# Optimization experiments

Measured on AMD Instinct MI355X. Metric: run time of the kernel, lower is better.

The kernel has to match this reference:

```python
import jax, jax.numpy as jnp
import numpy as np

N_NODES = 100000


def setup_inputs() -> dict:
    key = jax.random.key(0)
    k_x, k_r, k_c, k_v, k_t = jax.random.split(key, 5)
    n_edges = 3200000
    fin, fout = 512, 128
    x = jax.random.normal(k_x, (N_NODES, fin), dtype=jnp.float32)
    rows = jax.random.randint(k_r, (n_edges,), 0, N_NODES, dtype=jnp.int32)
    cols = jax.random.randint(k_c, (n_edges,), 0, N_NODES, dtype=jnp.int32)
    vals = jax.random.uniform(k_v, (n_edges,), dtype=jnp.float32)
    theta = jax.random.normal(k_t, (fin, fout), dtype=jnp.float32) * (1.0 / np.sqrt(fin))
    bias = jnp.zeros((fout,), dtype=jnp.float32)
    return {"x": x, "rows": rows, "cols": cols, "vals": vals, "theta": theta, "bias": bias}


def reference(x, rows, cols, vals, theta, bias):
    # SpMM: mx[i] = sum over edges (i <- j) of A[i,j] * x[j]
    gathered = vals[:, None] * x[cols]                      # [E, fin]
    mx = jax.ops.segment_sum(gathered, rows, num_segments=N_NODES)  # [N, fin]
    # Dense feature transform + bias + relu
    o = jnp.einsum('nf,fo->no', mx, theta) + bias           # [N, fout]
    return jax.nn.relu(o)
```

## Files before the change

### kernel.cpp

```cpp
#include <hip/hip_runtime.h>
#include <stdint.h>
#include <stddef.h>

#define FIN 512
#define FOUT 128
#define BROWS 160
#define NBK 625
#define SORT_CAP 7680
#define TILE 8192

typedef __attribute__((ext_vector_type(8))) short short8;
typedef __attribute__((ext_vector_type(4))) float f32x4;

__device__ __forceinline__ unsigned short f2bf(float f) {
  unsigned u = __builtin_bit_cast(unsigned, f);
  u = (u + 0x7fffu + ((u >> 16) & 1u)) >> 16;
  return (unsigned short)u;
}
__device__ __forceinline__ float bf2f(unsigned short h) {
  unsigned u = ((unsigned)h) << 16;
  return __builtin_bit_cast(float, u);
}

__global__ void prep_theta_k(const float* __restrict__ theta,
                             unsigned short* __restrict__ thetaT) {
  int idx = blockIdx.x * blockDim.x + threadIdx.x;
  int n = idx >> 9;
  int k = idx & 511;
  thetaT[idx] = f2bf(theta[k * FOUT + n]);
}

__global__ __launch_bounds__(256) void gemm_k(const float* __restrict__ x,
                                              const unsigned short* __restrict__ thetaT,
                                              unsigned short* __restrict__ yb, int M) {
  __shared__ __align__(16) unsigned short lA[128 * 40];
  __shared__ __align__(16) unsigned short lB[128 * 40];
  const int tid = threadIdx.x;
  const int row0 = blockIdx.x * 128;
  const int wave = tid >> 6, lane = tid & 63;
  const int wm = wave >> 1, wn = wave & 1;
  const int fr = lane & 15, fq = lane >> 4;
  const int arow = tid >> 1, ahalf = tid & 1;

  f32x4 acc[4][4] = {};

  const int grow = row0 + arow;
  const bool aval = (grow < M);
  const float* asrc = x + (size_t)(aval ? grow : 0) * FIN + ahalf * 16;
  const unsigned short* bsrc = thetaT + (size_t)arow * FIN + ahalf * 16;

  for (int k0 = 0; k0 < FIN; k0 += 32) {
    float av[16];
    if (aval) {
      const float4* p = (const float4*)(asrc + k0);
      float4 v0 = p[0], v1 = p[1], v2 = p[2], v3 = p[3];
      av[0] = v0.x; av[1] = v0.y; av[2] = v0.z; av[3] = v0.w;
      av[4] = v1.x; av[5] = v1.y; av[6] = v1.z; av[7] = v1.w;
      av[8] = v2.x; av[9] = v2.y; av[10] = v2.z; av[11] = v2.w;
      av[12] = v3.x; av[13] = v3.y; av[14] = v3.z; av[15] = v3.w;
    } else {
      for (int i = 0; i < 16; i++) av[i] = 0.f;
    }
    unsigned ap[8];
    for (int i = 0; i < 8; i++)
      ap[i] = (unsigned)f2bf(av[2 * i]) | ((unsigned)f2bf(av[2 * i + 1]) << 16);
    uint4* aw = (uint4*)&lA[arow * 40 + ahalf * 16];
    aw[0] = make_uint4(ap[0], ap[1], ap[2], ap[3]);
    aw[1] = make_uint4(ap[4], ap[5], ap[6], ap[7]);

    const uint4* bp = (const uint4*)(bsrc + k0);
    uint4 b0 = bp[0], b1 = bp[1];
    uint4* bw = (uint4*)&lB[arow * 40 + ahalf * 16];
    bw[0] = b0; bw[1] = b1;

    __syncthreads();

    short8 af[4], bfv[4];
#pragma unroll
    for (int m = 0; m < 4; m++)
      af[m] = *(const short8*)&lA[(wm * 64 + m * 16 + fr) * 40 + fq * 8];
#pragma unroll
    for (int n = 0; n < 4; n++)
      bfv[n] = *(const short8*)&lB[(wn * 64 + n * 16 + fr) * 40 + fq * 8];
#pragma unroll
    for (int m = 0; m < 4; m++)
#pragma unroll
      for (int n = 0; n < 4; n++)
        acc[m][n] = __builtin_amdgcn_mfma_f32_16x16x32_bf16(af[m], bfv[n], acc[m][n], 0, 0, 0);

    __syncthreads();
  }

#pragma unroll
  for (int m = 0; m < 4; m++) {
    int rbase = row0 + wm * 64 + m * 16 + fq * 4;
#pragma unroll
    for (int j = 0; j < 4; j++) {
      int r = rbase + j;
      if (r < M) {
        unsigned short* dst = yb + (size_t)r * FOUT + wn * 64;
#pragma unroll
        for (int n = 0; n < 4; n++) dst[n * 16 + fr] = f2bf(acc[m][n][j]);
      }
    }
  }
}

__global__ __launch_bounds__(256) void tilesort_k(const int* __restrict__ rows,
                                                  const int* __restrict__ cols,
                                                  const float* __restrict__ vals,
                                                  unsigned* __restrict__ rec4tile,
                                                  unsigned char* __restrict__ rlotile,
                                                  int* __restrict__ lofs, int E) {
  __shared__ int hist[NBK];
  __shared__ int wsum[4];
  __shared__ unsigned srec[TILE];
  __shared__ unsigned char srlo[TILE];
  const int c = blockIdx.x, t = threadIdx.x;
  const int base = c * TILE;
  const int n = (E - base < TILE) ? (E - base) : TILE;

  for (int i = t; i < NBK; i += 256) hist[i] = 0;
  __syncthreads();

#pragma unroll
  for (int k = 0; k < TILE / 256; k++) {
    int i = base + k * 256 + t;
    if (i < E) atomicAdd(&hist[rows[i] / BROWS], 1);
  }
  __syncthreads();

  int c0 = t * 3, c1 = c0 + 1, c2 = c0 + 2;
  int h0 = (c0 < NBK) ? hist[c0] : 0;
  int h1 = (c1 < NBK) ? hist[c1] : 0;
  int h2 = (c2 < NBK) ? hist[c2] : 0;
  int loc = h0 + h1 + h2;
  int lane = t & 63, wv = t >> 6;
  int inc = loc;
  for (int off = 1; off < 64; off <<= 1) {
    int u = __shfl_up(inc, off, 64);
    if (lane >= off) inc += u;
  }
  if (lane == 63) wsum[wv] = inc;
  __syncthreads();
  int excl = inc - loc;
  for (int i = 0; i < 4; i++)
    if (i < wv) excl += wsum[i];

  size_t lbase = (size_t)c * (NBK + 1);
  int e = excl;
  if (c0 <= NBK) lofs[lbase + c0] = e;
  __syncthreads();
  if (c0 < NBK) hist[c0] = e;
  e += h0;
  if (c1 <= NBK) lofs[lbase + c1] = e;
  if (c1 < NBK) hist[c1] = e;
  e += h1;
  if (c2 <= NBK) lofs[lbase + c2] = e;
  if (c2 < NBK) hist[c2] = e;
  __syncthreads();

#pragma unroll
  for (int k = 0; k < TILE / 256; k++) {
    int i = base + k * 256 + t;
    if (i < E) {
      int r = rows[i];
      int b = r / BROWS;
      int p = atomicAdd(&hist[b], 1);
      srec[p] = ((unsigned)cols[i] << 15) | ((unsigned)f2bf(vals[i]) & 0x7fffu);
      srlo[p] = (unsigned char)(r - b * BROWS);
    }
  }
  __syncthreads();

  for (int j = t; j < n; j += 256) {
    rec4tile[base + j] = srec[j];
    rlotile[base + j] = srlo[j];
  }
}

__global__ __launch_bounds__(256) void bsum_k(const int* __restrict__ lofs,
                                              int* __restrict__ btotals, int NT) {
  __shared__ int ws[4];
  int b = blockIdx.x, t = threadIdx.x;
  int s = 0;
  for (int c = t; c < NT; c += 256) {
    size_t lb = (size_t)c * (NBK + 1) + b;
    s += lofs[lb + 1] - lofs[lb];
  }
  for (int off = 32; off; off >>= 1) s += __shfl_down(s, off, 64);
  if ((t & 63) == 0) ws[t >> 6] = s;
  __syncthreads();
  if (t == 0) btotals[b] = ws[0] + ws[1] + ws[2] + ws[3];
}

__global__ __launch_bounds__(1024) void bscan_k(const int* __restrict__ btotals,
                                                int* __restrict__ boff,
                                                int* __restrict__ offsets,
                                                int E, int M) {
  __shared__ int tmp[1024];
  int t = threadIdx.x;
  tmp[t] = (t < NBK) ? btotals[t] : 0;
  __syncthreads();
  for (int off = 1; off < 1024; off <<= 1) {
    int v = (t >= off) ? tmp[t - off] : 0;
    __syncthreads();
    tmp[t] += v;
    __syncthreads();
  }
  if (t < NBK) boff[t] = t ? tmp[t - 1] : 0;
  if (t == 0) {
    boff[NBK] = E;
    offsets[M] = E;
  }
}

__global__ __launch_bounds__(256) void bsort_k(const int* __restrict__ boff,
                                               const int* __restrict__ lofs,
                                               const unsigned* __restrict__ rec4tile,
                                               const unsigned char* __restrict__ rlotile,
                                               unsigned* __restrict__ rec4s,
                                               int* __restrict__ offsets,
                                               int NT, int M) {
  __shared__ unsigned s4[SORT_CAP];
  __shared__ unsigned char k8[SORT_CAP];
  __shared__ int lh[256];
  __shared__ int lsc[256];
  __shared__ int wsum[4];
  int b = blockIdx.x, t = threadIdx.x;
  int start = boff[b];

  int ca = 2 * t, cb = 2 * t + 1;
  int la = 0, fa = 0, lb2 = 0, fb = 0;
  if (ca < NT) {
    size_t p = (size_t)ca * (NBK + 1) + b;
    la = lofs[p];
    fa = lofs[p + 1] - la;
  }
  if (cb < NT) {
    size_t p = (size_t)cb * (NBK + 1) + b;
    lb2 = lofs[p];
    fb = lofs[p + 1] - lb2;
  }
  int loc = fa + fb;
  int lane = t & 63, wv = t >> 6;
  int inc = loc;
  for (int off = 1; off < 64; off <<= 1) {
    int u = __shfl_up(inc, off, 64);
    if (lane >= off) inc += u;
  }
  if (lane == 63) wsum[wv] = inc;
  __syncthreads();
  int excl = inc - loc;
  for (int i = 0; i < 4; i++)
    if (i < wv) excl += wsum[i];

  if (ca < NT) {
    const unsigned* src = rec4tile + (size_t)ca * TILE + la;
    const unsigned char* srl = rlotile + (size_t)ca * TILE + la;
    for (int j = 0; j < fa; j++) {
      int d = excl + j;
      if (d < SORT_CAP) { s4[d] = src[j]; k8[d] = srl[j]; }
    }
    excl += fa;
  }
  if (cb < NT) {
    const unsigned* src = rec4tile + (size_t)cb * TILE + lb2;
    const unsigned char* srl = rlotile + (size_t)cb * TILE + lb2;
    for (int j = 0; j < fb; j++) {
      int d = excl + j;
      if (d < SORT_CAP) { s4[d] = src[j]; k8[d] = srl[j]; }
    }
  }

  int n = boff[b + 1] - start;
  if (n > SORT_CAP) n = SORT_CAP;
  lh[t] = 0;
  __syncthreads();

  for (int i = t; i < n; i += 256) atomicAdd(&lh[k8[i]], 1);
  __syncthreads();
  lsc[t] = lh[t];
  __syncthreads();
  for (int off = 1; off < 256; off <<= 1) {
    int v = (t >= off) ? lsc[t - off] : 0;
    __syncthreads();
    lsc[t] += v;
    __syncthreads();
  }
  int ex = t ? lsc[t - 1] : 0;
  int row = b * BROWS + t;
  if (t < BROWS && row < M) offsets[row] = start + ex;
  lh[t] = ex;
  __syncthreads();
  for (int i = t; i < n; i += 256) {
    unsigned r = s4[i];
    int p = atomicAdd(&lh[k8[i]], 1);
    rec4s[start + p] = r;
  }
}

__global__ __launch_bounds__(256) void rowv2_k(const int* __restrict__ offsets,
                                               const unsigned* __restrict__ rec4,
                                               const unsigned short* __restrict__ yb,
                                               const float* __restrict__ bias,
                                               float* __restrict__ out, int M) {
  int gid = blockIdx.x * blockDim.x + threadIdx.x;
  int r = gid >> 4;
  int l = gid & 15;
  if (r >= M) return;
  int s = offsets[r], e = offsets[r + 1];
  const unsigned short* src = yb + l * 8;

  float a0 = 0.f, a1 = 0.f, a2 = 0.f, a3 = 0.f, a4 = 0.f, a5 = 0.f, a6 = 0.f, a7 = 0.f;
  float c0 = 0.f, c1 = 0.f, c2 = 0.f, c3 = 0.f, c4 = 0.f, c5 = 0.f, c6 = 0.f, c7 = 0.f;

  int i = s;
  for (; i + 2 <= e; i += 2) {
    unsigned q0 = rec4[i];
    unsigned q1 = rec4[i + 1];
    const uint4 u0 = *(const uint4*)(src + (size_t)(q0 >> 15) * FOUT);
    const uint4 u1 = *(const uint4*)(src + (size_t)(q1 >> 15) * FOUT);
    float v0 = __builtin_bit_cast(float, (q0 & 0x7fffu) << 16);
    float v1 = __builtin_bit_cast(float, (q1 & 0x7fffu) << 16);
    a0 += v0 * __builtin_bit_cast(float, u0.x << 16);
    a1 += v0 * __builtin_bit_cast(float, u0.x & 0xffff0000u);
    a2 += v0 * __builtin_bit_cast(float, u0.y << 16);
    a3 += v0 * __builtin_bit_cast(float, u0.y & 0xffff0000u);
    a4 += v0 * __builtin_bit_cast(float, u0.z << 16);
    a5 += v0 * __builtin_bit_cast(float, u0.z & 0xffff0000u);
    a6 += v0 * __builtin_bit_cast(float, u0.w << 16);
    a7 += v0 * __builtin_bit_cast(float, u0.w & 0xffff0000u);
    c0 += v1 * __builtin_bit_cast(float, u1.x << 16);
    c1 += v1 * __builtin_bit_cast(float, u1.x & 0xffff0000u);
    c2 += v1 * __builtin_bit_cast(float, u1.y << 16);
    c3 += v1 * __builtin_bit_cast(float, u1.y & 0xffff0000u);
    c4 += v1 * __builtin_bit_cast(float, u1.z << 16);
    c5 += v1 * __builtin_bit_cast(float, u1.z & 0xffff0000u);
    c6 += v1 * __builtin_bit_cast(float, u1.w << 16);
    c7 += v1 * __builtin_bit_cast(float, u1.w & 0xffff0000u);
  }
  if (i < e) {
    unsigned q0 = rec4[i];
    const uint4 u0 = *(const uint4*)(src + (size_t)(q0 >> 15) * FOUT);
    float v0 = __builtin_bit_cast(float, (q0 & 0x7fffu) << 16);
    a0 += v0 * __builtin_bit_cast(float, u0.x << 16);
    a1 += v0 * __builtin_bit_cast(float, u0.x & 0xffff0000u);
    a2 += v0 * __builtin_bit_cast(float, u0.y << 16);
    a3 += v0 * __builtin_bit_cast(float, u0.y & 0xffff0000u);
    a4 += v0 * __builtin_bit_cast(float, u0.z << 16);
    a5 += v0 * __builtin_bit_cast(float, u0.z & 0xffff0000u);
    a6 += v0 * __builtin_bit_cast(float, u0.w << 16);
    a7 += v0 * __builtin_bit_cast(float, u0.w & 0xffff0000u);
  }

  const float4 b0 = *(const float4*)(bias + l * 8);
  const float4 b1 = *(const float4*)(bias + l * 8 + 4);
  float* dst = out + (size_t)r * FOUT + l * 8;
  float4 o0, o1;
  o0.x = fmaxf(a0 + c0 + b0.x, 0.f);
  o0.y = fmaxf(a1 + c1 + b0.y, 0.f);
  o0.z = fmaxf(a2 + c2 + b0.z, 0.f);
  o0.w = fmaxf(a3 + c3 + b0.w, 0.f);
  o1.x = fmaxf(a4 + c4 + b1.x, 0.f);
  o1.y = fmaxf(a5 + c5 + b1.y, 0.f);
  o1.z = fmaxf(a6 + c6 + b1.z, 0.f);
  o1.w = fmaxf(a7 + c7 + b1.w, 0.f);
  *(float4*)(dst) = o0;
  *(float4*)(dst + 4) = o1;
}

extern "C" void kernel_launch(void* const* d_in, const int* in_sizes, int n_in,
                              void* d_out, int out_size, void* d_ws, size_t ws_size,
                              hipStream_t stream) {
  const float* x = (const float*)d_in[0];
  const int* rows = (const int*)d_in[1];
  const int* cols = (const int*)d_in[2];
  const float* vals = (const float*)d_in[3];
  const float* theta = (const float*)d_in[4];
  const float* bias = (const float*)d_in[5];
  float* out = (float*)d_out;
  const int M = in_sizes[0] / FIN;
  const int E = in_sizes[1];
  const int NT = (E + TILE - 1) / TILE;

  char* w = (char*)d_ws;
  auto alloc = [&](size_t bytes) {
    char* p = w;
    w += (bytes + 255) & ~(size_t)255;
    return p;
  };
  unsigned short* yb = (unsigned short*)alloc((size_t)M * FOUT * 2);
  unsigned short* thetaT = (unsigned short*)alloc((size_t)FIN * FOUT * 2);
  unsigned* rec4tile = (unsigned*)alloc((size_t)NT * TILE * 4);
  unsigned char* rlotile = (unsigned char*)alloc((size_t)NT * TILE);
  int* lofs = (int*)alloc((size_t)NT * (NBK + 1) * 4);
  int* btotals = (int*)alloc((size_t)NBK * 4);
  int* boff = (int*)alloc((size_t)(NBK + 1) * 4);
  int* offsets = (int*)alloc((size_t)(M + 1) * 4);
  unsigned* rec4s = (unsigned*)alloc((size_t)E * 4);

  prep_theta_k<<<(FIN * FOUT) / 256, 256, 0, stream>>>(theta, thetaT);
  gemm_k<<<(M + 127) / 128, 256, 0, stream>>>(x, thetaT, yb, M);
  tilesort_k<<<NT, 256, 0, stream>>>(rows, cols, vals, rec4tile, rlotile, lofs, E);
  bsum_k<<<NBK, 256, 0, stream>>>(lofs, btotals, NT);
  bscan_k<<<1, 1024, 0, stream>>>(btotals, boff, offsets, E, M);
  bsort_k<<<NBK, 256, 0, stream>>>(boff, lofs, rec4tile, rlotile, rec4s, offsets, NT, M);
  rowv2_k<<<(M * 16 + 255) / 256, 256, 0, stream>>>(offsets, rec4s, yb, bias, out, M);
}
```

Measured before the change: 292.7 us.

## Fold bucket totals into tilesort via atomics and parallelize bsort fragment copy

```diff
diff --git a/kernel.cpp b/kernel.cpp
--- a/kernel.cpp
+++ b/kernel.cpp
@@ -8,6 +8,7 @@
 #define NBK 625
 #define SORT_CAP 7680
 #define TILE 8192
+#define MAXNT 512
 
 typedef __attribute__((ext_vector_type(8))) short short8;
 typedef __attribute__((ext_vector_type(4))) float f32x4;
@@ -111,7 +112,8 @@
                                                   const float* __restrict__ vals,
                                                   unsigned* __restrict__ rec4tile,
                                                   unsigned char* __restrict__ rlotile,
-                                                  int* __restrict__ lofs, int E) {
+                                                  int* __restrict__ lofs,
+                                                  int* __restrict__ btotals, int E) {
   __shared__ int hist[NBK];
   __shared__ int wsum[4];
   __shared__ unsigned srec[TILE];
@@ -134,6 +136,9 @@
   int h0 = (c0 < NBK) ? hist[c0] : 0;
   int h1 = (c1 < NBK) ? hist[c1] : 0;
   int h2 = (c2 < NBK) ? hist[c2] : 0;
+  if (h0) atomicAdd(&btotals[c0], h0);
+  if (h1) atomicAdd(&btotals[c1], h1);
+  if (h2) atomicAdd(&btotals[c2], h2);
   int loc = h0 + h1 + h2;
   int lane = t & 63, wv = t >> 6;
   int inc = loc;
@@ -177,21 +182,6 @@
     rec4tile[base + j] = srec[j];
     rlotile[base + j] = srlo[j];
   }
-}
-
-__global__ __launch_bounds__(256) void bsum_k(const int* __restrict__ lofs,
-                                              int* __restrict__ btotals, int NT) {
-  __shared__ int ws[4];
-  int b = blockIdx.x, t = threadIdx.x;
-  int s = 0;
-  for (int c = t; c < NT; c += 256) {
-    size_t lb = (size_t)c * (NBK + 1) + b;
-    s += lofs[lb + 1] - lofs[lb];
-  }
-  for (int off = 32; off; off >>= 1) s += __shfl_down(s, off, 64);
-  if ((t & 63) == 0) ws[t >> 6] = s;
-  __syncthreads();
-  if (t == 0) btotals[b] = ws[0] + ws[1] + ws[2] + ws[3];
 }
 
 __global__ __launch_bounds__(1024) void bscan_k(const int* __restrict__ btotals,
@@ -227,6 +217,9 @@
   __shared__ int lh[256];
   __shared__ int lsc[256];
   __shared__ int wsum[4];
+  __shared__ int fsrc[MAXNT];
+  __shared__ int fdst[MAXNT];
+  __shared__ int flen[MAXNT];
   int b = blockIdx.x, t = threadIdx.x;
   int start = boff[b];
 
@@ -256,26 +249,34 @@
     if (i < wv) excl += wsum[i];
 
   if (ca < NT) {
-    const unsigned* src = rec4tile + (size_t)ca * TILE + la;
-    const unsigned char* srl = rlotile + (size_t)ca * TILE + la;
-    for (int j = 0; j < fa; j++) {
-      int d = excl + j;
-      if (d < SORT_CAP) { s4[d] = src[j]; k8[d] = srl[j]; }
-    }
-    excl += fa;
+    fsrc[ca] = ca * TILE + la;
+    fdst[ca] = excl;
+    flen[ca] = fa;
   }
   if (cb < NT) {
-    const unsigned* src = rec4tile + (size_t)cb * TILE + lb2;
-    const unsigned char* srl = rlotile + (size_t)cb * TILE + lb2;
-    for (int j = 0; j < fb; j++) {
-      int d = excl + j;
-      if (d < SORT_CAP) { s4[d] = src[j]; k8[d] = srl[j]; }
+    fsrc[cb] = cb * TILE + lb2;
+    fdst[cb] = excl + fa;
+    flen[cb] = fb;
+  }
+  lh[t] = 0;
+  __syncthreads();
+
+  int grp = t >> 4, l16 = t & 15;
+  for (int f = grp; f < NT; f += 16) {
+    int L = flen[f];
+    int sd = fdst[f];
+    int ss = fsrc[f];
+    for (int j = l16; j < L; j += 16) {
+      int d = sd + j;
+      if (d < SORT_CAP) {
+        s4[d] = rec4tile[ss + j];
+        k8[d] = rlotile[ss + j];
+      }
     }
   }
 
   int n = boff[b + 1] - start;
   if (n > SORT_CAP) n = SORT_CAP;
-  lh[t] = 0;
   __syncthreads();
 
   for (int i = t; i < n; i += 256) atomicAdd(&lh[k8[i]], 1);
@@ -400,10 +401,10 @@
   int* offsets = (int*)alloc((size_t)(M + 1) * 4);
   unsigned* rec4s = (unsigned*)alloc((size_t)E * 4);
 
+  hipMemsetAsync(btotals, 0, (size_t)NBK * 4, stream);
   prep_theta_k<<<(FIN * FOUT) / 256, 256, 0, stream>>>(theta, thetaT);
   gemm_k<<<(M + 127) / 128, 256, 0, stream>>>(x, thetaT, yb, M);
-  tilesort_k<<<NT, 256, 0, stream>>>(rows, cols, vals, rec4tile, rlotile, lofs, E);
-  bsum_k<<<NBK, 256, 0, stream>>>(lofs, btotals, NT);
+  tilesort_k<<<NT, 256, 0, stream>>>(rows, cols, vals, rec4tile, rlotile, lofs, btotals, E);
   bscan_k<<<1, 1024, 0, stream>>>(btotals, boff, offsets, E, M);
   bsort_k<<<NBK, 256, 0, stream>>>(boff, lofs, rec4tile, rlotile, rec4s, offsets, NT, M);
   rowv2_k<<<(M * 16 + 255) / 256, 256, 0, stream>>>(offsets, rec4s, yb, bias, out, M);
```

Result: no change. 294.9 us (+0.7%).
